# Performance work log

Measured on AMD Instinct MI355X. Metric: run time of the kernel, lower is better.

## Reference

```python
import jax, jax.numpy as jnp
import numpy as np

N = 4096          # num_nodes
U = 2048          # num_users
R = 5             # num_relations
B = 30            # num_bases
H0 = 500          # hidden_size[0]
H1 = 75           # hidden_size[1]
E = 262144        # num_edges
EPS = 1e-5


def setup_inputs() -> dict:
    key = jax.random.key(0)
    ks = jax.random.split(key, 10)
    x = jax.random.normal(ks[0], (N, N), dtype=jnp.float32)
    edge_index = jax.random.randint(ks[1], (2, E), 0, N, dtype=jnp.int64)
    edge_type = jax.random.randint(ks[2], (E,), 0, R, dtype=jnp.int64)
    # RGCNConv basis-decomposition parameters
    basis = jax.random.normal(ks[3], (B, N, H0), dtype=jnp.float32) * 0.02
    comp = jax.random.normal(ks[4], (R, B), dtype=jnp.float32) * 0.1
    root = jax.random.normal(ks[5], (N, H0), dtype=jnp.float32) * 0.02
    bias_rgcn = jnp.zeros((H0,), dtype=jnp.float32)
    # DenseLayer (Linear without bias) + BatchNorm1d affine params
    fc_w = jax.random.normal(ks[6], (H1, H0), dtype=jnp.float32) * 0.05
    bn_gamma_u = jnp.ones((U,), dtype=jnp.float32)
    bn_beta_u = jnp.zeros((U,), dtype=jnp.float32)
    bn_gamma_i = jnp.ones((N - U,), dtype=jnp.float32)
    bn_beta_i = jnp.zeros((N - U,), dtype=jnp.float32)
    return {
        "x": x, "basis": basis, "comp": comp, "root": root,
        "bias_rgcn": bias_rgcn, "fc_w": fc_w,
        "bn_gamma_u": bn_gamma_u, "bn_beta_u": bn_beta_u,
        "bn_gamma_i": bn_gamma_i, "bn_beta_i": bn_beta_i,
        "edge_index": edge_index, "edge_type": edge_type,
    }


def _bn1d(z, gamma, beta):
    # BatchNorm1d applied to z.unsqueeze(0): channels = rows, normalize over feature dim
    mu = z.mean(axis=1, keepdims=True)
    var = ((z - mu) ** 2).mean(axis=1, keepdims=True)
    return gamma[:, None] * (z - mu) / jnp.sqrt(var + EPS) + beta[:, None]


def _forward(x, basis, comp, root, bias_rgcn, fc_w,
             bn_gamma_u, bn_beta_u, bn_gamma_i, bn_beta_i,
             edge_index, edge_type):
    # --- RGCNConv with basis decomposition, mean aggregation per relation ---
    W = jnp.einsum('rb,bio->rio', comp, basis)          # [R, N, H0]
    h = jnp.einsum('ni,rio->rno', x, W)                 # [R, N, H0] transformed feats
    src, dst = edge_index[0], edge_index[1]
    msgs = h[edge_type, src]                            # [E, H0] gather
    seg = dst * R + edge_type                           # (target, relation) segments
    sums = jax.ops.segment_sum(msgs, seg, num_segments=N * R)
    cnt = jax.ops.segment_sum(jnp.ones((E,), dtype=msgs.dtype), seg, num_segments=N * R)
    agg = (sums / jnp.maximum(cnt, 1.0)[:, None]).reshape(N, R, H0).sum(axis=1)
    feats = agg + x @ root + bias_rgcn                  # [N, H0]

    # --- separate (accum != 'stack') ---
    u, i = feats[:U], feats[U:]

    # --- DenseLayer: dropout (eval: identity) -> Linear(no bias) -> BN -> ReLU ---
    u = jax.nn.relu(_bn1d(u @ fc_w.T, bn_gamma_u, bn_beta_u))
    i = jax.nn.relu(_bn1d(i @ fc_w.T, bn_gamma_i, bn_beta_i))
    return u, i


def reference(x, basis, comp, root, bias_rgcn, fc_w,
              bn_gamma_u, bn_beta_u, bn_gamma_i, bn_beta_i,
              edge_index, edge_type):
    return _forward(x, basis, comp, root, bias_rgcn, fc_w,
                    bn_gamma_u, bn_beta_u, bn_gamma_i, bn_beta_i,
                    edge_index, edge_type)
```

## Files before the change

### kernel.cpp

```cpp
#include <hip/hip_runtime.h>
#include <hip/hip_bf16.h>
#include <stdint.h>

#define N_NODES 4096
#define U_NODES 2048
#define R_REL 5
#define B_BASES 30
#define H0 500
#define H1 75
#define E_EDGES 262144
#define EPS_BN 1e-5f
#define K_DIM 4096
#define M_COLS 3000
#define M_PAD 3072
#define NSEG (N_NODES*R_REL)

typedef __attribute__((ext_vector_type(4))) float f32x4;
typedef __attribute__((ext_vector_type(8))) short bf16x8;

static __device__ __forceinline__ ushort bf16_bits(float f) {
    union { float f; uint32_t u; } c; c.f = f;
    uint32_t u = c.u;
    uint32_t r = (u + 0x7fffu + ((u >> 16) & 1u)) >> 16;
    return (ushort)r;
}

static __device__ __forceinline__ float bf16_to_f(ushort u) {
    union { uint32_t u; float f; } c; c.u = ((uint32_t)u) << 16; return c.f;
}

static __device__ __forceinline__ void async_copy16(const ushort* g, ushort* l) {
    __builtin_amdgcn_global_load_lds((const __attribute__((address_space(1))) void*)g,
                                     (__attribute__((address_space(3))) void*)l,
                                     16, 0, 0);
}

__global__ void k_convert_x(const float* __restrict__ x, ushort* __restrict__ xb) {
    int i = (blockIdx.x * 256 + threadIdx.x) * 4;
    float4 v = *(const float4*)(x + i);
    ushort4 o;
    o.x = bf16_bits(v.x); o.y = bf16_bits(v.y);
    o.z = bf16_bits(v.z); o.w = bf16_bits(v.w);
    *(ushort4*)(xb + i) = o;
}

__global__ void k_make_wallT(const float* __restrict__ basis, const float* __restrict__ comp,
                             const float* __restrict__ root, ushort* __restrict__ wallT) {
    __shared__ float compl_[R_REL * B_BASES];
    __shared__ float T[32][33];
    int t = threadIdx.x;
    if (t < R_REL * B_BASES) compl_[t] = comp[t];
    __syncthreads();
    int k0 = blockIdx.x * 32, o0 = blockIdx.y * 32;
    int o_in = t & 31, k_in = t >> 5;
    int o = o0 + o_in;
    bool ov = (o < H0);
    float acc[4][6];
    #pragma unroll
    for (int a = 0; a < 4; a++)
        #pragma unroll
        for (int r = 0; r < 6; r++) acc[a][r] = 0.f;
    for (int b = 0; b < B_BASES; b++) {
        float cw[5];
        #pragma unroll
        for (int r = 0; r < 5; r++) cw[r] = compl_[r * B_BASES + b];
        #pragma unroll
        for (int a = 0; a < 4; a++) {
            int k = k0 + a * 8 + k_in;
            float v = ov ? basis[(size_t)b * K_DIM * H0 + (size_t)k * H0 + o] : 0.f;
            #pragma unroll
            for (int r = 0; r < 5; r++) acc[a][r] += cw[r] * v;
        }
    }
    #pragma unroll
    for (int a = 0; a < 4; a++) {
        int k = k0 + a * 8 + k_in;
        acc[a][5] = ov ? root[(size_t)k * H0 + o] : 0.f;
    }
    for (int r = 0; r < 6; r++) {
        __syncthreads();
        #pragma unroll
        for (int a = 0; a < 4; a++) T[o_in][a * 8 + k_in] = acc[a][r];
        __syncthreads();
        int ro = t >> 5, ck = t & 31;
        #pragma unroll
        for (int a = 0; a < 4; a++) {
            int oo = ro + a * 8;
            int om = o0 + oo;
            if (om < H0) {
                int m = r * H0 + om;
                wallT[(size_t)m * K_DIM + k0 + ck] = bf16_bits(T[oo][ck]);
            }
        }
    }
}

__global__ __launch_bounds__(256) void k_gemm(const ushort* __restrict__ A,
                                              const ushort* __restrict__ BT,
                                              ushort* __restrict__ C) {
    __shared__ __align__(16) ushort As[128 * 64];
    __shared__ __align__(16) ushort Bs[128 * 64];
    int tid = threadIdx.x;
    int lane = tid & 63, wave = tid >> 6;
    int m0 = blockIdx.x * 128, n0 = blockIdx.y * 128;
    int wm = (wave & 1) * 64, wn = (wave >> 1) * 64;

    f32x4 acc[4][4];
    #pragma unroll
    for (int a = 0; a < 4; a++)
        #pragma unroll
        for (int b = 0; b < 4; b++) { f32x4 z = {0.f, 0.f, 0.f, 0.f}; acc[a][b] = z; }

    int srow = tid >> 3;
    int skc = (((tid & 7) ^ ((tid >> 3) & 7))) * 8;
    const ushort* Abase = A + (size_t)(m0 + srow) * K_DIM + skc;
    const ushort* Bbase = BT + (size_t)(n0 + srow) * K_DIM + skc;
    int ldsoff = (wave * 64) * 8;

    for (int k0 = 0; k0 < K_DIM; k0 += 64) {
        const ushort* ga = Abase + k0;
        const ushort* gb = Bbase + k0;
        #pragma unroll
        for (int i = 0; i < 4; i++) {
            async_copy16(ga + (size_t)i * 32 * K_DIM, As + i * 2048 + ldsoff);
            async_copy16(gb + (size_t)i * 32 * K_DIM, Bs + i * 2048 + ldsoff);
        }
        __syncthreads();
        #pragma unroll
        for (int kk = 0; kk < 64; kk += 32) {
            bf16x8 af[4], bfr[4];
            int koff = kk + ((lane >> 4) * 8);
            int g = koff >> 3;
            #pragma unroll
            for (int a = 0; a < 4; a++) {
                int row = wm + a * 16 + (lane & 15);
                int sw = (g ^ (row & 7)) * 8;
                af[a] = *(const bf16x8*)(As + row * 64 + sw);
            }
            #pragma unroll
            for (int b = 0; b < 4; b++) {
                int row = wn + b * 16 + (lane & 15);
                int sw = (g ^ (row & 7)) * 8;
                bfr[b] = *(const bf16x8*)(Bs + row * 64 + sw);
            }
            #pragma unroll
            for (int a = 0; a < 4; a++)
                #pragma unroll
                for (int b = 0; b < 4; b++)
                    acc[a][b] = __builtin_amdgcn_mfma_f32_16x16x32_bf16(af[a], bfr[b], acc[a][b], 0, 0, 0);
        }
        __syncthreads();
    }

    int col = lane & 15;
    int rbase = (lane >> 4) * 4;
    #pragma unroll
    for (int a = 0; a < 4; a++) {
        #pragma unroll
        for (int b = 0; b < 4; b++) {
            int gn = n0 + wn + b * 16 + col;
            if (gn < M_COLS) {
                #pragma unroll
                for (int r = 0; r < 4; r++) {
                    int gm = m0 + wm + a * 16 + rbase + r;
                    C[(size_t)gm * M_COLS + gn] = bf16_bits(acc[a][b][r]);
                }
            }
        }
    }
}

__global__ void k_count(const int* __restrict__ ei, const int* __restrict__ et, int* __restrict__ cnt) {
    int e = blockIdx.x * 256 + threadIdx.x;
    if (e < E_EDGES) {
        int dst = ei[E_EDGES + e];
        int r = et[e];
        atomicAdd(&cnt[dst * R_REL + r], 1);
    }
}

__global__ void k_scan(const int* __restrict__ cnt, int* __restrict__ offs, int* __restrict__ cursor) {
    __shared__ int part[256];
    int t = threadIdx.x;
    const int CH = NSEG / 256;
    int s = 0;
    for (int i = 0; i < CH; i++) s += cnt[t * CH + i];
    part[t] = s;
    __syncthreads();
    for (int d = 1; d < 256; d <<= 1) {
        int v = (t >= d) ? part[t - d] : 0;
        __syncthreads();
        part[t] += v;
        __syncthreads();
    }
    int run = part[t] - s;
    for (int i = 0; i < CH; i++) {
        int idx = t * CH + i;
        offs[idx] = run;
        cursor[idx] = run;
        run += cnt[idx];
    }
    if (t == 255) offs[NSEG] = run;
}

__global__ void k_fill(const int* __restrict__ ei, const int* __restrict__ et,
                       int* __restrict__ cursor, int* __restrict__ edge_src) {
    int e = blockIdx.x * 256 + threadIdx.x;
    if (e < E_EDGES) {
        int src = ei[e];
        int dst = ei[E_EDGES + e];
        int r = et[e];
        int pos = atomicAdd(&cursor[dst * R_REL + r], 1);
        edge_src[pos] = src;
    }
}

__global__ void k_agg(const ushort* __restrict__ C, const int* __restrict__ offs,
                      const int* __restrict__ edge_src, const float* __restrict__ bias,
                      float* __restrict__ feats) {
    int n = blockIdx.x;
    int t = threadIdx.x;
    if (t >= 125) return;
    f32x4 acc = {0.f, 0.f, 0.f, 0.f};
    #pragma unroll
    for (int r = 0; r < R_REL; r++) {
        int seg = n * R_REL + r;
        int beg = offs[seg], end = offs[seg + 1];
        if (end > beg) {
            f32x4 s = {0.f, 0.f, 0.f, 0.f};
            for (int e = beg; e < end; e++) {
                int src = edge_src[e];
                ushort4 v = *(const ushort4*)(C + (size_t)src * M_COLS + r * H0 + t * 4);
                s.x += bf16_to_f(v.x); s.y += bf16_to_f(v.y);
                s.z += bf16_to_f(v.z); s.w += bf16_to_f(v.w);
            }
            float inv = 1.0f / (float)(end - beg);
            acc += s * inv;
        }
    }
    {
        ushort4 v = *(const ushort4*)(C + (size_t)n * M_COLS + 5 * H0 + t * 4);
        acc.x += bf16_to_f(v.x); acc.y += bf16_to_f(v.y);
        acc.z += bf16_to_f(v.z); acc.w += bf16_to_f(v.w);
    }
    acc += *(const f32x4*)(bias + t * 4);
    *(f32x4*)(feats + (size_t)n * H0 + t * 4) = acc;
}

__global__ __launch_bounds__(128) void k_fc_bn(const float* __restrict__ feats, const float* __restrict__ fcw,
                                               const float* __restrict__ gu, const float* __restrict__ bu,
                                               const float* __restrict__ gi, const float* __restrict__ bi,
                                               float* __restrict__ out) {
    __shared__ float fs[4][H0];
    __shared__ float z[4][80];
    int t = threadIdx.x;
    int row0 = blockIdx.x * 4;
    if (t < 125) {
        #pragma unroll
        for (int r = 0; r < 4; r++)
            *(f32x4*)&fs[r][t * 4] = *(const f32x4*)(feats + (size_t)(row0 + r) * H0 + t * 4);
    }
    __syncthreads();
    if (t < H1) {
        float a0 = 0.f, a1 = 0.f, a2 = 0.f, a3 = 0.f;
        const float* wr = fcw + (size_t)t * H0;
        for (int k = 0; k < H0; k += 4) {
            float4 w = *(const float4*)(wr + k);
            a0 += w.x * fs[0][k] + w.y * fs[0][k+1] + w.z * fs[0][k+2] + w.w * fs[0][k+3];
            a1 += w.x * fs[1][k] + w.y * fs[1][k+1] + w.z * fs[1][k+2] + w.w * fs[1][k+3];
            a2 += w.x * fs[2][k] + w.y * fs[2][k+1] + w.z * fs[2][k+2] + w.w * fs[2][k+3];
            a3 += w.x * fs[3][k] + w.y * fs[3][k+1] + w.z * fs[3][k+2] + w.w * fs[3][k+3];
        }
        z[0][t] = a0; z[1][t] = a1; z[2][t] = a2; z[3][t] = a3;
    }
    __syncthreads();
    int lane = t & 63, wave = t >> 6;
    #pragma unroll
    for (int rr = 0; rr < 2; rr++) {
        int r = wave * 2 + rr;
        int row = row0 + r;
        float a = (lane < H1) ? z[r][lane] : 0.f;
        float b2 = (lane < H1 - 64) ? z[r][64 + lane] : 0.f;
        float s1 = a + b2, s2 = a * a + b2 * b2;
        #pragma unroll
        for (int s = 32; s > 0; s >>= 1) { s1 += __shfl_xor(s1, s); s2 += __shfl_xor(s2, s); }
        float mean = s1 / (float)H1;
        float var = s2 / (float)H1 - mean * mean;
        float inv = 1.0f / sqrtf(var + EPS_BN);
        float gamma, beta;
        if (row < U_NODES) { gamma = gu[row];            beta = bu[row]; }
        else               { gamma = gi[row - U_NODES];  beta = bi[row - U_NODES]; }
        if (lane < H1) {
            float v = gamma * (a - mean) * inv + beta;
            out[(size_t)row * H1 + lane] = v > 0.f ? v : 0.f;
        }
        if (lane < H1 - 64) {
            float v = gamma * (b2 - mean) * inv + beta;
            out[(size_t)row * H1 + 64 + lane] = v > 0.f ? v : 0.f;
        }
    }
}

extern "C" void kernel_launch(void* const* d_in, const int* in_sizes, int n_in,
                              void* d_out, int out_size, void* d_ws, size_t ws_size,
                              hipStream_t stream) {
    (void)in_sizes; (void)n_in; (void)out_size; (void)ws_size;
    const float* x         = (const float*)d_in[0];
    const float* basis     = (const float*)d_in[1];
    const float* comp      = (const float*)d_in[2];
    const float* root      = (const float*)d_in[3];
    const float* bias_rgcn = (const float*)d_in[4];
    const float* fc_w      = (const float*)d_in[5];
    const float* gu        = (const float*)d_in[6];
    const float* bu        = (const float*)d_in[7];
    const float* gi        = (const float*)d_in[8];
    const float* bi        = (const float*)d_in[9];
    const int*   ei        = (const int*)d_in[10];
    const int*   et        = (const int*)d_in[11];
    float* out = (float*)d_out;

    char* ws = (char*)d_ws;
    size_t off = 0;
    auto carve = [&](size_t bytes) -> void* {
        void* p = ws + off;
        off += (bytes + 255) & ~(size_t)255;
        return p;
    };
    ushort* xb      = (ushort*)carve((size_t)N_NODES * K_DIM * 2);
    ushort* wallT   = (ushort*)carve((size_t)M_PAD * K_DIM * 2);
    ushort* hall    = (ushort*)carve((size_t)N_NODES * M_COLS * 2);
    float*  feats   = (float*) carve((size_t)N_NODES * H0 * 4);
    int*    cnt     = (int*)   carve((size_t)NSEG * 4);
    int*    offs    = (int*)   carve((size_t)(NSEG + 1) * 4);
    int*    cursor  = (int*)   carve((size_t)NSEG * 4);
    int*    edge_src= (int*)   carve((size_t)E_EDGES * 4);

    hipMemsetAsync(cnt, 0, NSEG * 4, stream);
    k_convert_x<<<16384, 256, 0, stream>>>(x, xb);
    k_make_wallT<<<dim3(128, 16), 256, 0, stream>>>(basis, comp, root, wallT);
    k_count<<<E_EDGES / 256, 256, 0, stream>>>(ei, et, cnt);
    k_scan<<<1, 256, 0, stream>>>(cnt, offs, cursor);
    k_fill<<<E_EDGES / 256, 256, 0, stream>>>(ei, et, cursor, edge_src);
    k_gemm<<<dim3(32, 24), 256, 0, stream>>>(xb, wallT, hall);
    k_agg<<<N_NODES, 128, 0, stream>>>(hall, offs, edge_src, bias_rgcn, feats);
    k_fc_bn<<<N_NODES / 4, 128, 0, stream>>>(feats, fc_w, gu, bu, gi, bi, out);
}
```

Measured before the change: 627.1 us.

## Fuse memset, remap GEMM blocks per XCD, vectorize scan, flatten aggregation loop

Zeroing of the count buffer moves into the x-conversion kernel, so the separate memset call goes away. The GEMM grid is flattened and blocks are remapped so each XCD works on a contiguous set of N tiles, which should improve L2 reuse. The scan reads and writes counts as int4 vectors. The fill kernel precomputes a packed (src, relation) index and a per-edge mean weight, which lets aggregation walk every edge of a node in one loop with four independent accumulators and gain more memory-level parallelism. The cost is an extra per-edge weight array and a different float summation order.

Measured after the change: 624.0 us. Within noise of the previous version (-0.5%).

```diff
diff --git a/kernel.cpp b/kernel.cpp
--- a/kernel.cpp
+++ b/kernel.cpp
@@ -29,14 +29,22 @@
     union { uint32_t u; float f; } c; c.u = ((uint32_t)u) << 16; return c.f;
 }
 
+static __device__ __forceinline__ void fma_u4(f32x4& s, float w, ushort4 v) {
+    s.x += w * bf16_to_f(v.x); s.y += w * bf16_to_f(v.y);
+    s.z += w * bf16_to_f(v.z); s.w += w * bf16_to_f(v.w);
+}
+
 static __device__ __forceinline__ void async_copy16(const ushort* g, ushort* l) {
     __builtin_amdgcn_global_load_lds((const __attribute__((address_space(1))) void*)g,
                                      (__attribute__((address_space(3))) void*)l,
                                      16, 0, 0);
 }
 
-__global__ void k_convert_x(const float* __restrict__ x, ushort* __restrict__ xb) {
-    int i = (blockIdx.x * 256 + threadIdx.x) * 4;
+__global__ void k_convert_x(const float* __restrict__ x, ushort* __restrict__ xb,
+                            int* __restrict__ cnt) {
+    int gid = blockIdx.x * 256 + threadIdx.x;
+    if (gid < NSEG) cnt[gid] = 0;
+    int i = gid * 4;
     float4 v = *(const float4*)(x + i);
     ushort4 o;
     o.x = bf16_bits(v.x); o.y = bf16_bits(v.y);
@@ -102,7 +110,12 @@
     __shared__ __align__(16) ushort Bs[128 * 64];
     int tid = threadIdx.x;
     int lane = tid & 63, wave = tid >> 6;
-    int m0 = blockIdx.x * 128, n0 = blockIdx.y * 128;
+    int bid = blockIdx.x;
+    int xcd = bid & 7;
+    int j = bid >> 3;
+    int n_t = xcd * 3 + (j >> 5);
+    int m_t = j & 31;
+    int m0 = m_t * 128, n0 = n_t * 128;
     int wm = (wave & 1) * 64, wn = (wave >> 1) * 64;
 
     f32x4 acc[4][4];
@@ -182,9 +195,11 @@
 __global__ void k_scan(const int* __restrict__ cnt, int* __restrict__ offs, int* __restrict__ cursor) {
     __shared__ int part[256];
     int t = threadIdx.x;
-    const int CH = NSEG / 256;
+    int4 buf[20];
+    const int4* c4 = (const int4*)(cnt + t * 80);
     int s = 0;
-    for (int i = 0; i < CH; i++) s += cnt[t * CH + i];
+    #pragma unroll
+    for (int i = 0; i < 20; i++) { buf[i] = c4[i]; s += buf[i].x + buf[i].y + buf[i].z + buf[i].w; }
     part[t] = s;
     __syncthreads();
     for (int d = 1; d < 256; d <<= 1) {
@@ -194,50 +209,62 @@
         __syncthreads();
     }
     int run = part[t] - s;
-    for (int i = 0; i < CH; i++) {
-        int idx = t * CH + i;
-        offs[idx] = run;
-        cursor[idx] = run;
-        run += cnt[idx];
+    int4* o4 = (int4*)(offs + t * 80);
+    int4* u4 = (int4*)(cursor + t * 80);
+    #pragma unroll
+    for (int i = 0; i < 20; i++) {
+        int4 c = buf[i];
+        int4 o;
+        o.x = run; o.y = run + c.x; o.z = run + c.x + c.y; o.w = run + c.x + c.y + c.z;
+        run += c.x + c.y + c.z + c.w;
+        o4[i] = o; u4[i] = o;
     }
     if (t == 255) offs[NSEG] = run;
 }
 
 __global__ void k_fill(const int* __restrict__ ei, const int* __restrict__ et,
-                       int* __restrict__ cursor, int* __restrict__ edge_src) {
+                       const int* __restrict__ offs, int* __restrict__ cursor,
+                       int* __restrict__ edge_val, float* __restrict__ edge_w) {
     int e = blockIdx.x * 256 + threadIdx.x;
     if (e < E_EDGES) {
         int src = ei[e];
         int dst = ei[E_EDGES + e];
         int r = et[e];
-        int pos = atomicAdd(&cursor[dst * R_REL + r], 1);
-        edge_src[pos] = src;
+        int seg = dst * R_REL + r;
+        int pos = atomicAdd(&cursor[seg], 1);
+        edge_val[pos] = (src << 3) | r;
+        edge_w[pos] = 1.0f / (float)(offs[seg + 1] - offs[seg]);
     }
 }
 
 __global__ void k_agg(const ushort* __restrict__ C, const int* __restrict__ offs,
-                      const int* __restrict__ edge_src, const float* __restrict__ bias,
-                      float* __restrict__ feats) {
+                      const int* __restrict__ edge_val, const float* __restrict__ edge_w,
+                      const float* __restrict__ bias, float* __restrict__ feats) {
     int n = blockIdx.x;
     int t = threadIdx.x;
     if (t >= 125) return;
-    f32x4 acc = {0.f, 0.f, 0.f, 0.f};
-    #pragma unroll
-    for (int r = 0; r < R_REL; r++) {
-        int seg = n * R_REL + r;
-        int beg = offs[seg], end = offs[seg + 1];
-        if (end > beg) {
-            f32x4 s = {0.f, 0.f, 0.f, 0.f};
-            for (int e = beg; e < end; e++) {
-                int src = edge_src[e];
-                ushort4 v = *(const ushort4*)(C + (size_t)src * M_COLS + r * H0 + t * 4);
-                s.x += bf16_to_f(v.x); s.y += bf16_to_f(v.y);
-                s.z += bf16_to_f(v.z); s.w += bf16_to_f(v.w);
-            }
-            float inv = 1.0f / (float)(end - beg);
-            acc += s * inv;
-        }
-    }
+    int beg = offs[n * R_REL];
+    int end = offs[n * R_REL + R_REL];
+    f32x4 s0 = {0.f,0.f,0.f,0.f}, s1 = {0.f,0.f,0.f,0.f};
+    f32x4 s2 = {0.f,0.f,0.f,0.f}, s3 = {0.f,0.f,0.f,0.f};
+    const ushort* Ct = C + t * 4;
+    int e = beg;
+    for (; e + 3 < end; e += 4) {
+        int   v0 = edge_val[e],   v1 = edge_val[e+1], v2 = edge_val[e+2], v3 = edge_val[e+3];
+        float w0 = edge_w[e],     w1 = edge_w[e+1],   w2 = edge_w[e+2],   w3 = edge_w[e+3];
+        ushort4 a0 = *(const ushort4*)(Ct + (size_t)(v0 >> 3) * M_COLS + (v0 & 7) * H0);
+        ushort4 a1 = *(const ushort4*)(Ct + (size_t)(v1 >> 3) * M_COLS + (v1 & 7) * H0);
+        ushort4 a2 = *(const ushort4*)(Ct + (size_t)(v2 >> 3) * M_COLS + (v2 & 7) * H0);
+        ushort4 a3 = *(const ushort4*)(Ct + (size_t)(v3 >> 3) * M_COLS + (v3 & 7) * H0);
+        fma_u4(s0, w0, a0); fma_u4(s1, w1, a1); fma_u4(s2, w2, a2); fma_u4(s3, w3, a3);
+    }
+    for (; e < end; e++) {
+        int v = edge_val[e];
+        float w = edge_w[e];
+        ushort4 a = *(const ushort4*)(Ct + (size_t)(v >> 3) * M_COLS + (v & 7) * H0);
+        fma_u4(s0, w, a);
+    }
+    f32x4 acc = (s0 + s1) + (s2 + s3);
     {
         ushort4 v = *(const ushort4*)(C + (size_t)n * M_COLS + 5 * H0 + t * 4);
         acc.x += bf16_to_f(v.x); acc.y += bf16_to_f(v.y);
@@ -333,15 +360,15 @@
     int*    cnt     = (int*)   carve((size_t)NSEG * 4);
     int*    offs    = (int*)   carve((size_t)(NSEG + 1) * 4);
     int*    cursor  = (int*)   carve((size_t)NSEG * 4);
-    int*    edge_src= (int*)   carve((size_t)E_EDGES * 4);
-
-    hipMemsetAsync(cnt, 0, NSEG * 4, stream);
-    k_convert_x<<<16384, 256, 0, stream>>>(x, xb);
+    int*    edge_val= (int*)   carve((size_t)E_EDGES * 4);
+    float*  edge_w  = (float*) carve((size_t)E_EDGES * 4);
+
+    k_convert_x<<<16384, 256, 0, stream>>>(x, xb, cnt);
     k_make_wallT<<<dim3(128, 16), 256, 0, stream>>>(basis, comp, root, wallT);
     k_count<<<E_EDGES / 256, 256, 0, stream>>>(ei, et, cnt);
     k_scan<<<1, 256, 0, stream>>>(cnt, offs, cursor);
-    k_fill<<<E_EDGES / 256, 256, 0, stream>>>(ei, et, cursor, edge_src);
-    k_gemm<<<dim3(32, 24), 256, 0, stream>>>(xb, wallT, hall);
-    k_agg<<<N_NODES, 128, 0, stream>>>(hall, offs, edge_src, bias_rgcn, feats);
+    k_fill<<<E_EDGES / 256, 256, 0, stream>>>(ei, et, offs, cursor, edge_val, edge_w);
+    k_gemm<<<768, 256, 0, stream>>>(xb, wallT, hall);
+    k_agg<<<N_NODES, 128, 0, stream>>>(hall, offs, edge_val, edge_w, bias_rgcn, feats);
     k_fc_bn<<<N_NODES / 4, 128, 0, stream>>>(feats, fc_w, gu, bu, gi, bi, out);
 }
```
